# Kernel tuning notes

Measured on AMD Instinct MI355X. Metric: run time of the kernel, lower is better.

Reference implementation:

```python
import jax, jax.numpy as jnp
import numpy as np

B, SQ, SK, D = 16, 2048, 2048, 64


def setup_inputs() -> dict:
    key = jax.random.key(0)
    k1, k2, k3, k4 = jax.random.split(key, 4)
    return {
        "query": jax.random.normal(k1, (B, SQ, D), dtype=jnp.float32),
        "key": jax.random.normal(k2, (B, SK, D), dtype=jnp.float32),
        "value": jax.random.normal(k3, (B, SK, D), dtype=jnp.float32),
        "mask": jax.random.randint(k4, (B, SQ, SK), 0, 2).astype(bool),
    }


def reference(query, key, value, mask):
    # score = Q K^T / sqrt(D); masked positions -> -inf
    scale = 1.0 / jnp.sqrt(jnp.asarray(query.shape[-1], query.dtype))
    score = jnp.einsum("bqd,bkd->bqk", query, key) * scale  # [B, SQ, SK]
    score = jnp.where(mask, -jnp.inf, score)
    attn = jax.nn.softmax(score, axis=-1)
    context = jnp.einsum("bqk,bkd->bqd", attn, value)  # [B, SQ, D]
    return (context, attn)
```

## Files before the change

### kernel.cpp

```cpp
#include <hip/hip_runtime.h>
#include <hip/hip_bf16.h>

typedef __attribute__((ext_vector_type(8))) __bf16   bf16x8;
typedef __attribute__((ext_vector_type(4))) _Float16 f16x4;
typedef __attribute__((ext_vector_type(8))) _Float16 f16x8;
typedef __attribute__((ext_vector_type(4))) float    f32x4;
typedef __attribute__((ext_vector_type(4))) int      i32x4;
typedef __attribute__((ext_vector_type(8))) unsigned short u16x8;

namespace {
constexpr int kB   = 16;
constexpr int kSQ  = 2048;
constexpr int kSK  = 2048;
constexpr int kD   = 64;
constexpr int kQB  = 16;
constexpr int kNW  = 4;
constexpr int kTPW = 32;
constexpr int kNT  = kSK / 16;
constexpr int kCStride = 68;
constexpr float kScaleLog2e = 0.18033688011112042f;
constexpr size_t kKpElems = (size_t)kB * kNT * 2 * 64 * 8;
constexpr size_t kVpOff   = kKpElems * 2;
}

__global__ __launch_bounds__(256)
void conv_k(const float* __restrict__ K, unsigned short* __restrict__ Kp)
{
  const int idx = blockIdx.x * 256 + threadIdx.x;
  const int lam = idx & 63, f = (idx >> 6) & 1, kt = (idx >> 7) & (kNT - 1),
            b = idx >> 14;
  const int l15 = lam & 15, kg = lam >> 4;
  const float* src = K + ((size_t)(b * kSK + kt * 16 + l15) * kD) + f * 32 + kg * 8;
  u16x8 o;
#pragma unroll
  for (int e = 0; e < 8; ++e) {
    union { float f; unsigned int u; } cv; cv.f = src[e];
    unsigned int r = cv.u + 0x7fff + ((cv.u >> 16) & 1);
    o[e] = (unsigned short)(r >> 16);
  }
  *reinterpret_cast<u16x8*>(Kp + (size_t)idx * 8) = o;
}

__global__ __launch_bounds__(256)
void conv_v(const float* __restrict__ V, _Float16* __restrict__ Vp)
{
  const int idx = blockIdx.x * 256 + threadIdx.x;
  const int h = idx & 1, lam = (idx >> 1) & 63, t = (idx >> 7) & (kNT - 1),
            b = idx >> 14;
  const int l15 = lam & 15, kg = lam >> 4;
  f16x8 o;
#pragma unroll
  for (int j = 0; j < 2; ++j)
#pragma unroll
    for (int e = 0; e < 4; ++e)
      o[j * 4 + e] = (_Float16)
          V[((size_t)(b * kSK + t * 16 + kg * 4 + e) * kD) + (2 * h + j) * 16 + l15];
  *reinterpret_cast<f16x8*>(Vp + (size_t)idx * 8) = o;
}

__global__ __launch_bounds__(256, 3)
void sdpa_main(const float* __restrict__ Qg, const unsigned short* __restrict__ Kp,
               const _Float16* __restrict__ Vp, const int* __restrict__ Mg,
               float* __restrict__ ctxOut, float* __restrict__ attnOut)
{
  __shared__ float sums[kNW][kQB];
  __shared__ __align__(16) float cpart[kNW][kQB][kCStride];
  __shared__ __align__(16) char stg[kNW * 2048];

  const int tid  = threadIdx.x;
  const int wid  = tid >> 6;
  const int lane = tid & 63;
  const int l15  = lane & 15;
  const int kg   = lane >> 4;

  const int wg = (blockIdx.x & 7) * 256 + (blockIdx.x >> 3);
  const int b  = wg >> 7;
  const int q0 = (wg & 127) * kQB;

  const float* Qb = Qg + (size_t)b * kSQ * kD;
  const int qrow  = q0 + l15;
  const int kbase = wid * (kTPW * 16);
  const int gt0   = wid * kTPW;

  const unsigned short* Kpb = Kp + (size_t)b * kNT * 2 * 64 * 8;
  const _Float16*       Vpb = Vp + (size_t)b * kNT * 64 * 16;
  const int* mrow = Mg + (size_t)b * kSQ * kSK + (size_t)qrow * kSK + kbase;

  bf16x8 qf0, qf1;
  {
    const float* qp = Qb + (size_t)qrow * kD + kg * 8;
#pragma unroll
    for (int e = 0; e < 8; ++e) { qf0[e] = (__bf16)qp[e]; qf1[e] = (__bf16)qp[32 + e]; }
  }

  auto kfrag = [&](int t, int f) {
    return *reinterpret_cast<const bf16x8*>(
        Kpb + (((size_t)(gt0 + t) * 2 + f) * 64 + lane) * 8);
  };

  f16x4 pb[kTPW];
  float lsum = 0.f;
  i32x4 mbuf[6];
  bf16x8 kb0[2], kb1[2];
#pragma unroll
  for (int p = 0; p < 6; ++p)
    mbuf[p] = *reinterpret_cast<const i32x4*>(mrow + p * 16 + kg * 4);
  kb0[0] = kfrag(0, 0); kb1[0] = kfrag(0, 1);
#pragma unroll
  for (int t = 0; t < kTPW; ++t) {
    const int cur = t & 1, nxt = cur ^ 1;
    if (t + 1 < kTPW) { kb0[nxt] = kfrag(t + 1, 0); kb1[nxt] = kfrag(t + 1, 1); }
    f32x4 acc = {0.f, 0.f, 0.f, 0.f};
    acc = __builtin_amdgcn_mfma_f32_16x16x32_bf16(kb0[cur], qf0, acc, 0, 0, 0);
    acc = __builtin_amdgcn_mfma_f32_16x16x32_bf16(kb1[cur], qf1, acc, 0, 0, 0);
    const i32x4 mv = mbuf[t % 6];
    if (t + 6 < kTPW)
      mbuf[t % 6] = *reinterpret_cast<const i32x4*>(mrow + (t + 6) * 16 + kg * 4);
    f16x4 p4;
#pragma unroll
    for (int r = 0; r < 4; ++r) {
      const float pv = mv[r] ? 0.f : __builtin_amdgcn_exp2f(acc[r] * kScaleLog2e);
      lsum += pv;
      p4[r] = (_Float16)pv;
    }
    pb[t] = p4;
  }
  lsum += __shfl_xor(lsum, 16, 64);
  lsum += __shfl_xor(lsum, 32, 64);
  if (lane < 16) sums[wid][l15] = lsum;
  __syncthreads();

  {
    const int r0 = lane >> 3, r1 = r0 + 8;
    float la = 0.f, lb = 0.f;
#pragma unroll
    for (int w = 0; w < kNW; ++w) { la += sums[w][r0]; lb += sums[w][r1]; }
    const float invA = 1.0f / la, invB = 1.0f / lb;
    char* sw = stg + wid * 2048;
    const int cb = (lane & 7) * 16;
    float* arow0 = attnOut + ((size_t)b * kSQ + q0 + r0) * kSK + kbase + (lane & 7) * 8;
    float* arow1 = attnOut + ((size_t)b * kSQ + q0 + r1) * kSK + kbase + (lane & 7) * 8;
#pragma unroll
    for (int g = 0; g < 8; ++g) {
#pragma unroll
      for (int tl = 0; tl < 4; ++tl) {
        const int byte = (l15 * 128 + tl * 32 + kg * 8) ^ ((l15 & 7) << 4);
        *reinterpret_cast<f16x4*>(sw + byte) = pb[g * 4 + tl];
      }
      const f16x8 x0 = *reinterpret_cast<const f16x8*>(
          sw + ((r0 * 128 + cb) ^ ((r0 & 7) << 4)));
      const f16x8 x1 = *reinterpret_cast<const f16x8*>(
          sw + ((r1 * 128 + cb) ^ ((r1 & 7) << 4)));
      float4 o0a, o0b, o1a, o1b;
      o0a.x = (float)x0[0] * invA; o0a.y = (float)x0[1] * invA;
      o0a.z = (float)x0[2] * invA; o0a.w = (float)x0[3] * invA;
      o0b.x = (float)x0[4] * invA; o0b.y = (float)x0[5] * invA;
      o0b.z = (float)x0[6] * invA; o0b.w = (float)x0[7] * invA;
      o1a.x = (float)x1[0] * invB; o1a.y = (float)x1[1] * invB;
      o1a.z = (float)x1[2] * invB; o1a.w = (float)x1[3] * invB;
      o1b.x = (float)x1[4] * invB; o1b.y = (float)x1[5] * invB;
      o1b.z = (float)x1[6] * invB; o1b.w = (float)x1[7] * invB;
      *reinterpret_cast<float4*>(arow0 + g * 64)     = o0a;
      *reinterpret_cast<float4*>(arow0 + g * 64 + 4) = o0b;
      *reinterpret_cast<float4*>(arow1 + g * 64)     = o1a;
      *reinterpret_cast<float4*>(arow1 + g * 64 + 4) = o1b;
    }
  }

  f32x4 cacc[4];
#pragma unroll
  for (int d = 0; d < 4; ++d) cacc[d] = f32x4{0.f, 0.f, 0.f, 0.f};
#pragma unroll
  for (int t = 0; t < kTPW; ++t) {
    const f16x4 pfrag = pb[t];
    const _Float16* vb = Vpb + ((size_t)(gt0 + t) * 64 + lane) * 16;
    union { f16x8 v; f16x4 h[2]; } u01, u23;
    u01.v = *reinterpret_cast<const f16x8*>(vb);
    u23.v = *reinterpret_cast<const f16x8*>(vb + 8);
    cacc[0] = __builtin_amdgcn_mfma_f32_16x16x16f16(u01.h[0], pfrag, cacc[0], 0, 0, 0);
    cacc[1] = __builtin_amdgcn_mfma_f32_16x16x16f16(u01.h[1], pfrag, cacc[1], 0, 0, 0);
    cacc[2] = __builtin_amdgcn_mfma_f32_16x16x16f16(u23.h[0], pfrag, cacc[2], 0, 0, 0);
    cacc[3] = __builtin_amdgcn_mfma_f32_16x16x16f16(u23.h[1], pfrag, cacc[3], 0, 0, 0);
  }
#pragma unroll
  for (int dblk = 0; dblk < 4; ++dblk)
    *reinterpret_cast<f32x4*>(&cpart[wid][l15][dblk * 16 + kg * 4]) = cacc[dblk];
  __syncthreads();

  {
    const int q = tid >> 4;
    const int d = (tid & 15) * 4;
    float4 o = make_float4(0.f, 0.f, 0.f, 0.f);
#pragma unroll
    for (int w = 0; w < kNW; ++w) {
      const float4 p = *reinterpret_cast<const float4*>(&cpart[w][q][d]);
      o.x += p.x; o.y += p.y; o.z += p.z; o.w += p.w;
    }
    float l = 0.f;
#pragma unroll
    for (int w = 0; w < kNW; ++w) l += sums[w][q];
    const float iv = 1.0f / l;
    o.x *= iv; o.y *= iv; o.z *= iv; o.w *= iv;
    *reinterpret_cast<float4*>(ctxOut + ((size_t)b * kSQ + q0 + q) * kD + d) = o;
  }
}

extern "C" void kernel_launch(void* const* d_in, const int* in_sizes, int n_in,
                              void* d_out, int out_size, void* d_ws, size_t ws_size,
                              hipStream_t stream)
{
  const float* Q = (const float*)d_in[0];
  const float* K = (const float*)d_in[1];
  const float* V = (const float*)d_in[2];
  const int*   M = (const int*)d_in[3];
  float* ctx  = (float*)d_out;
  float* attn = (float*)d_out + (size_t)kB * kSQ * kD;

  unsigned short* Kp = (unsigned short*)d_ws;
  _Float16*       Vp = (_Float16*)((char*)d_ws + kVpOff);

  hipLaunchKernelGGL(conv_k, dim3(1024), dim3(256), 0, stream, K, Kp);
  hipLaunchKernelGGL(conv_v, dim3(1024), dim3(256), 0, stream, V, Vp);
  hipLaunchKernelGGL(sdpa_main, dim3(kB * kSQ / kQB), dim3(256), 0, stream,
                     Q, Kp, Vp, M, ctx, attn);
}
```

Before: 195.8 us.

## Pack int mask into bitmask in a pre-pass, pad attn staging, double-buffer V

Adds a conv_m pre-kernel that uses wave ballots to compress the int32 mask into a 1-bit-per-element bitmask in workspace. The main kernel then loads 16 mask words per lane up front instead of streaming int32 mask vectors during the QK loop. The attention-output staging in LDS switches from an XOR swizzle to a padded row stride, and V fragments are now double-buffered in the PV loop. The full mask is still read once, but in a separate serial pass, so the main kernel can no longer overlap mask reads with compute, and the extra launch adds overhead.

```diff
diff --git a/kernel.cpp b/kernel.cpp
--- a/kernel.cpp
+++ b/kernel.cpp
@@ -18,9 +18,10 @@
 constexpr int kTPW = 32;
 constexpr int kNT  = kSK / 16;
 constexpr int kCStride = 68;
+constexpr int kStgStride = 144;
 constexpr float kScaleLog2e = 0.18033688011112042f;
-constexpr size_t kKpElems = (size_t)kB * kNT * 2 * 64 * 8;
-constexpr size_t kVpOff   = kKpElems * 2;
+constexpr size_t kVpOff   = 4u << 20;
+constexpr size_t kBitsOff = 8u << 20;
 }
 
 __global__ __launch_bounds__(256)
@@ -58,14 +59,31 @@
   *reinterpret_cast<f16x8*>(Vp + (size_t)idx * 8) = o;
 }
 
+__global__ __launch_bounds__(256)
+void conv_m(const int* __restrict__ M, unsigned long long* __restrict__ bits)
+{
+  const int gtid = blockIdx.x * 256 + threadIdx.x;
+  const int wv   = gtid >> 6;
+  const int lane = gtid & 63;
+  const size_t ibase = (size_t)wv * 4096;
+  unsigned long long myword = 0;
+#pragma unroll
+  for (int j = 0; j < 64; ++j) {
+    const int v = M[ibase + (size_t)j * 64 + lane];
+    const unsigned long long bb = __ballot(v != 0);
+    myword = (lane == j) ? bb : myword;
+  }
+  bits[(size_t)wv * 64 + lane] = myword;
+}
+
 __global__ __launch_bounds__(256, 3)
 void sdpa_main(const float* __restrict__ Qg, const unsigned short* __restrict__ Kp,
-               const _Float16* __restrict__ Vp, const int* __restrict__ Mg,
+               const _Float16* __restrict__ Vp, const unsigned int* __restrict__ Mbits,
                float* __restrict__ ctxOut, float* __restrict__ attnOut)
 {
   __shared__ float sums[kNW][kQB];
   __shared__ __align__(16) float cpart[kNW][kQB][kCStride];
-  __shared__ __align__(16) char stg[kNW * 2048];
+  __shared__ __align__(16) char stg[kNW * kQB * kStgStride];
 
   const int tid  = threadIdx.x;
   const int wid  = tid >> 6;
@@ -84,13 +102,24 @@
 
   const unsigned short* Kpb = Kp + (size_t)b * kNT * 2 * 64 * 8;
   const _Float16*       Vpb = Vp + (size_t)b * kNT * 64 * 16;
-  const int* mrow = Mg + (size_t)b * kSQ * kSK + (size_t)qrow * kSK + kbase;
 
   bf16x8 qf0, qf1;
   {
     const float* qp = Qb + (size_t)qrow * kD + kg * 8;
 #pragma unroll
     for (int e = 0; e < 8; ++e) { qf0[e] = (__bf16)qp[e]; qf1[e] = (__bf16)qp[32 + e]; }
+  }
+
+  unsigned int mw[16];
+  {
+    const unsigned int* mwp = Mbits + ((size_t)(b * kSQ + qrow) * (kSK / 32))
+                                     + (kbase >> 5);
+#pragma unroll
+    for (int i = 0; i < 4; ++i) {
+      const i32x4 v = *reinterpret_cast<const i32x4*>(mwp + i * 4);
+#pragma unroll
+      for (int j = 0; j < 4; ++j) mw[i * 4 + j] = (unsigned int)v[j];
+    }
   }
 
   auto kfrag = [&](int t, int f) {
@@ -100,11 +129,7 @@
 
   f16x4 pb[kTPW];
   float lsum = 0.f;
-  i32x4 mbuf[6];
   bf16x8 kb0[2], kb1[2];
-#pragma unroll
-  for (int p = 0; p < 6; ++p)
-    mbuf[p] = *reinterpret_cast<const i32x4*>(mrow + p * 16 + kg * 4);
   kb0[0] = kfrag(0, 0); kb1[0] = kfrag(0, 1);
 #pragma unroll
   for (int t = 0; t < kTPW; ++t) {
@@ -113,13 +138,14 @@
     f32x4 acc = {0.f, 0.f, 0.f, 0.f};
     acc = __builtin_amdgcn_mfma_f32_16x16x32_bf16(kb0[cur], qf0, acc, 0, 0, 0);
     acc = __builtin_amdgcn_mfma_f32_16x16x32_bf16(kb1[cur], qf1, acc, 0, 0, 0);
-    const i32x4 mv = mbuf[t % 6];
-    if (t + 6 < kTPW)
-      mbuf[t % 6] = *reinterpret_cast<const i32x4*>(mrow + (t + 6) * 16 + kg * 4);
+    const unsigned int bits4 =
+        (mw[t >> 1] >> (((t & 1) << 4) + (kg << 2))) & 15u;
     f16x4 p4;
 #pragma unroll
     for (int r = 0; r < 4; ++r) {
-      const float pv = mv[r] ? 0.f : __builtin_amdgcn_exp2f(acc[r] * kScaleLog2e);
+      const float pv = ((bits4 >> r) & 1u)
+                           ? 0.f
+                           : __builtin_amdgcn_exp2f(acc[r] * kScaleLog2e);
       lsum += pv;
       p4[r] = (_Float16)pv;
     }
@@ -136,51 +162,61 @@
 #pragma unroll
     for (int w = 0; w < kNW; ++w) { la += sums[w][r0]; lb += sums[w][r1]; }
     const float invA = 1.0f / la, invB = 1.0f / lb;
-    char* sw = stg + wid * 2048;
-    const int cb = (lane & 7) * 16;
-    float* arow0 = attnOut + ((size_t)b * kSQ + q0 + r0) * kSK + kbase + (lane & 7) * 8;
-    float* arow1 = attnOut + ((size_t)b * kSQ + q0 + r1) * kSK + kbase + (lane & 7) * 8;
+    char* sw = stg + wid * (kQB * kStgStride);
+    const int c8 = (lane & 7) * 8;
+    float* arow0 = attnOut + ((size_t)b * kSQ + q0 + r0) * kSK + kbase;
+    float* arow1 = attnOut + ((size_t)b * kSQ + q0 + r1) * kSK + kbase;
 #pragma unroll
     for (int g = 0; g < 8; ++g) {
 #pragma unroll
-      for (int tl = 0; tl < 4; ++tl) {
-        const int byte = (l15 * 128 + tl * 32 + kg * 8) ^ ((l15 & 7) << 4);
-        *reinterpret_cast<f16x4*>(sw + byte) = pb[g * 4 + tl];
-      }
-      const f16x8 x0 = *reinterpret_cast<const f16x8*>(
-          sw + ((r0 * 128 + cb) ^ ((r0 & 7) << 4)));
-      const f16x8 x1 = *reinterpret_cast<const f16x8*>(
-          sw + ((r1 * 128 + cb) ^ ((r1 & 7) << 4)));
-      float4 o0a, o0b, o1a, o1b;
-      o0a.x = (float)x0[0] * invA; o0a.y = (float)x0[1] * invA;
-      o0a.z = (float)x0[2] * invA; o0a.w = (float)x0[3] * invA;
-      o0b.x = (float)x0[4] * invA; o0b.y = (float)x0[5] * invA;
-      o0b.z = (float)x0[6] * invA; o0b.w = (float)x0[7] * invA;
-      o1a.x = (float)x1[0] * invB; o1a.y = (float)x1[1] * invB;
-      o1a.z = (float)x1[2] * invB; o1a.w = (float)x1[3] * invB;
-      o1b.x = (float)x1[4] * invB; o1b.y = (float)x1[5] * invB;
-      o1b.z = (float)x1[6] * invB; o1b.w = (float)x1[7] * invB;
-      *reinterpret_cast<float4*>(arow0 + g * 64)     = o0a;
-      *reinterpret_cast<float4*>(arow0 + g * 64 + 4) = o0b;
-      *reinterpret_cast<float4*>(arow1 + g * 64)     = o1a;
-      *reinterpret_cast<float4*>(arow1 + g * 64 + 4) = o1b;
+      for (int tl = 0; tl < 4; ++tl)
+        *reinterpret_cast<f16x4*>(sw + l15 * kStgStride + tl * 32 + kg * 8)
+            = pb[g * 4 + tl];
+      const f16x4 x0a = *reinterpret_cast<const f16x4*>(sw + r0 * kStgStride + c8);
+      const f16x4 x0b = *reinterpret_cast<const f16x4*>(sw + r0 * kStgStride + 64 + c8);
+      const f16x4 x1a = *reinterpret_cast<const f16x4*>(sw + r1 * kStgStride + c8);
+      const f16x4 x1b = *reinterpret_cast<const f16x4*>(sw + r1 * kStgStride + 64 + c8);
+      float4 o;
+      const int cA = g * 64 + (lane & 7) * 4;
+      o.x = (float)x0a[0] * invA; o.y = (float)x0a[1] * invA;
+      o.z = (float)x0a[2] * invA; o.w = (float)x0a[3] * invA;
+      *reinterpret_cast<float4*>(arow0 + cA) = o;
+      o.x = (float)x0b[0] * invA; o.y = (float)x0b[1] * invA;
+      o.z = (float)x0b[2] * invA; o.w = (float)x0b[3] * invA;
+      *reinterpret_cast<float4*>(arow0 + cA + 32) = o;
+      o.x = (float)x1a[0] * invB; o.y = (float)x1a[1] * invB;
+      o.z = (float)x1a[2] * invB; o.w = (float)x1a[3] * invB;
+      *reinterpret_cast<float4*>(arow1 + cA) = o;
+      o.x = (float)x1b[0] * invB; o.y = (float)x1b[1] * invB;
+      o.z = (float)x1b[2] * invB; o.w = (float)x1b[3] * invB;
+      *reinterpret_cast<float4*>(arow1 + cA + 32) = o;
     }
   }
 
   f32x4 cacc[4];
 #pragma unroll
   for (int d = 0; d < 4; ++d) cacc[d] = f32x4{0.f, 0.f, 0.f, 0.f};
+  f16x8 v01[2], v23[2];
+  {
+    const _Float16* vb = Vpb + ((size_t)gt0 * 64 + lane) * 16;
+    v01[0] = *reinterpret_cast<const f16x8*>(vb);
+    v23[0] = *reinterpret_cast<const f16x8*>(vb + 8);
+  }
 #pragma unroll
   for (int t = 0; t < kTPW; ++t) {
+    const int cur = t & 1, nxt = cur ^ 1;
+    if (t + 1 < kTPW) {
+      const _Float16* vb = Vpb + ((size_t)(gt0 + t + 1) * 64 + lane) * 16;
+      v01[nxt] = *reinterpret_cast<const f16x8*>(vb);
+      v23[nxt] = *reinterpret_cast<const f16x8*>(vb + 8);
+    }
     const f16x4 pfrag = pb[t];
-    const _Float16* vb = Vpb + ((size_t)(gt0 + t) * 64 + lane) * 16;
-    union { f16x8 v; f16x4 h[2]; } u01, u23;
-    u01.v = *reinterpret_cast<const f16x8*>(vb);
-    u23.v = *reinterpret_cast<const f16x8*>(vb + 8);
-    cacc[0] = __builtin_amdgcn_mfma_f32_16x16x16f16(u01.h[0], pfrag, cacc[0], 0, 0, 0);
-    cacc[1] = __builtin_amdgcn_mfma_f32_16x16x16f16(u01.h[1], pfrag, cacc[1], 0, 0, 0);
-    cacc[2] = __builtin_amdgcn_mfma_f32_16x16x16f16(u23.h[0], pfrag, cacc[2], 0, 0, 0);
-    cacc[3] = __builtin_amdgcn_mfma_f32_16x16x16f16(u23.h[1], pfrag, cacc[3], 0, 0, 0);
+    union { f16x8 v; f16x4 h[2]; } a, c;
+    a.v = v01[cur]; c.v = v23[cur];
+    cacc[0] = __builtin_amdgcn_mfma_f32_16x16x16f16(a.h[0], pfrag, cacc[0], 0, 0, 0);
+    cacc[1] = __builtin_amdgcn_mfma_f32_16x16x16f16(a.h[1], pfrag, cacc[1], 0, 0, 0);
+    cacc[2] = __builtin_amdgcn_mfma_f32_16x16x16f16(c.h[0], pfrag, cacc[2], 0, 0, 0);
+    cacc[3] = __builtin_amdgcn_mfma_f32_16x16x16f16(c.h[1], pfrag, cacc[3], 0, 0, 0);
   }
 #pragma unroll
   for (int dblk = 0; dblk < 4; ++dblk)
@@ -216,11 +252,13 @@
   float* ctx  = (float*)d_out;
   float* attn = (float*)d_out + (size_t)kB * kSQ * kD;
 
-  unsigned short* Kp = (unsigned short*)d_ws;
-  _Float16*       Vp = (_Float16*)((char*)d_ws + kVpOff);
+  unsigned short*     Kp = (unsigned short*)d_ws;
+  _Float16*           Vp = (_Float16*)((char*)d_ws + kVpOff);
+  unsigned long long* Mb = (unsigned long long*)((char*)d_ws + kBitsOff);
 
   hipLaunchKernelGGL(conv_k, dim3(1024), dim3(256), 0, stream, K, Kp);
   hipLaunchKernelGGL(conv_v, dim3(1024), dim3(256), 0, stream, V, Vp);
+  hipLaunchKernelGGL(conv_m, dim3(4096), dim3(256), 0, stream, M, Mb);
   hipLaunchKernelGGL(sdpa_main, dim3(kB * kSQ / kQB), dim3(256), 0, stream,
-                     Q, Kp, Vp, M, ctx, attn);
-}
+                     Q, Kp, Vp, (const unsigned int*)Mb, ctx, attn);
+}
```

New measurement: 185.4 us. 1.06x faster.
